# Kernel optimization log

Hardware: AMD Instinct MI355X
Metric: run time of the kernel (lower is better)

Reference implementation:

```python
import jax, jax.numpy as jnp
import numpy as np

LEAKY = 0.1  # leaky_hmm_coefficient (pychain default)


def _fb_objf(x_exp, tfrom, tto, tpdf, tprob, init_p, final_p):
    """Leaky-HMM forward recursion for one sequence.
    x_exp: [T, P] exp'd nnet outputs; transitions are edge lists of length E.
    Returns scalar log-prob of the sequence under the graph.
    """
    S = init_p.shape[0]

    def step(carry, obs):
        alpha, logz = carry  # alpha: [S] normalized occupation probs
        # per-edge contribution: alpha[src] * trans_prob * obs[pdf]
        contrib = alpha[tfrom] * tprob * obs[tpdf]          # [E]
        new_alpha = jnp.zeros(S, alpha.dtype).at[tto].add(contrib)
        tot = new_alpha.sum()
        # leaky-HMM: redistribute a fraction of total mass via initial probs
        new_alpha = new_alpha + LEAKY * tot * init_p
        scale = new_alpha.sum()
        return (new_alpha / scale, logz + jnp.log(scale)), None

    (alpha_T, logz), _ = jax.lax.scan(step, (init_p, jnp.zeros((), x_exp.dtype)), x_exp)
    return logz + jnp.log(jnp.sum(alpha_T * final_p))


def setup_inputs() -> dict:
    key = jax.random.key(0)
    ks = jax.random.split(key, 12)
    B, T, P = 32, 500, 3000
    S_den, E_den = 2000, 40000
    S_num, E_num = 100, 400

    x = jax.random.normal(ks[0], (B, T, P), jnp.float32)

    # denominator graph (shared across batch); every state gets incoming arcs
    den_to = (jnp.arange(E_den, dtype=jnp.int32) % S_den)
    den_from = jax.random.randint(ks[1], (E_den,), 0, S_den, jnp.int32)
    den_pdf = jax.random.randint(ks[2], (E_den,), 0, P, jnp.int32)
    den_prob = jax.random.uniform(ks[3], (E_den,), jnp.float32, 0.1, 1.0)
    den_init = jax.random.uniform(ks[4], (S_den,), jnp.float32, 0.1, 1.0)
    den_init = den_init / den_init.sum()
    den_final = jax.random.uniform(ks[5], (S_den,), jnp.float32, 0.1, 1.0)

    # numerator graphs (one per utterance), batched edge lists
    num_to = jnp.tile(jnp.arange(E_num, dtype=jnp.int32) % S_num, (B, 1))
    num_from = jax.random.randint(ks[6], (B, E_num), 0, S_num, jnp.int32)
    num_pdf = jax.random.randint(ks[7], (B, E_num), 0, P, jnp.int32)
    num_prob = jax.random.uniform(ks[8], (B, E_num), jnp.float32, 0.1, 1.0)
    num_init = jax.random.uniform(ks[9], (B, S_num), jnp.float32, 0.1, 1.0)
    num_init = num_init / num_init.sum(axis=1, keepdims=True)
    num_final = jax.random.uniform(ks[10], (B, S_num), jnp.float32, 0.1, 1.0)

    return {
        "x": x,
        "den_from": den_from, "den_to": den_to, "den_pdf": den_pdf,
        "den_prob": den_prob, "den_init": den_init, "den_final": den_final,
        "num_from": num_from, "num_to": num_to, "num_pdf": num_pdf,
        "num_prob": num_prob, "num_init": num_init, "num_final": num_final,
    }


def reference(x, den_from, den_to, den_pdf, den_prob, den_init, den_final,
              num_from, num_to, num_pdf, num_prob, num_init, num_final):
    B, T, _ = x.shape
    exp_x = jnp.exp(jnp.clip(x, -30.0, 30.0))  # [B, T, P]

    # denominator: shared graph across batch
    den_objf = jax.vmap(_fb_objf, in_axes=(0, None, None, None, None, None, None))(
        exp_x, den_from, den_to, den_pdf, den_prob, den_init, den_final).sum()
    # numerator: per-utterance graph
    num_objf = jax.vmap(_fb_objf, in_axes=(0, 0, 0, 0, 0, 0, 0))(
        exp_x, num_from, num_to, num_pdf, num_prob, num_init, num_final).sum()

    objf = -(num_objf - den_objf)
    return objf / (B * T)  # avg=True
```

## Files before the change

kernel.cpp:

```cpp
#include <hip/hip_runtime.h>


#define LEAKY 0.1f
#define AGENT __HIP_MEMORY_SCOPE_AGENT

constexpr int B = 32, T = 500, P = 3000;
constexpr int S_DEN = 2000;
constexpr int S_NUM = 100, E_NUM = 400;
constexpr int NTH = 1024;
constexpr int NWAVE = NTH / 64;
constexpr int G_DEN = 5;
constexpr int SB = S_DEN / G_DEN;
constexpr int KE = 20;
constexpr int EPT = KE / 2;
constexpr int OBS_T0 = 800;
constexpr int OBS_N = NTH - OBS_T0;
constexpr int OBS_IT = (P + OBS_N - 1) / OBS_N;
constexpr int KE_NUM = 4;
constexpr int NDEN_BLK = B * G_DEN;


__device__ __forceinline__ float clampexp(float x) {
  return __expf(fminf(fmaxf(x, -30.f), 30.f));
}
__device__ __forceinline__ void st_f32(float* p, float v) {
  __hip_atomic_store(p, v, __ATOMIC_RELAXED, AGENT);
}
__device__ __forceinline__ unsigned long long ld_u64(const float* p) {
  return __hip_atomic_load((const unsigned long long*)p, __ATOMIC_RELAXED,
                           AGENT);
}

__device__ __forceinline__ float reduce_1024(float v, float* wpart) {
#pragma unroll
  for (int off = 32; off; off >>= 1) v += __shfl_xor(v, off, 64);
  if ((threadIdx.x & 63) == 0) wpart[threadIdx.x >> 6] = v;
  __syncthreads();
  float s = 0.f;
#pragma unroll
  for (int w = 0; w < NWAVE; ++w) s += wpart[w];
  return s;
}

__device__ void run_den(const float* __restrict__ xb,
                        const int* __restrict__ ef_g,
                        const int* __restrict__ ep_g,
                        const float* __restrict__ epr_g,
                        const float* __restrict__ einit,
                        const float* __restrict__ efinal, int b, int g,
                        float* __restrict__ outs, float* __restrict__ parts_b,
                        float* obsA, float* obsB, float* cur, float* ini_s,
                        float* wpart) {
  const int tid = threadIdx.x;
  const int lane = tid & 63;
  const bool gat = tid < 2 * SB;
  const bool cons = tid < S_DEN / 2;
  const int jloc = (tid >> 6) * 32 + (lane >> 1);
  const int half = lane & 1;
  const int j = g * SB + jloc;

  float lsum = 0.f;
  if (cons) {
    const float2 iv = ((const float2*)einit)[tid];
    ((float2*)ini_s)[tid] = iv;
    lsum = iv.x + iv.y;
  }
  __syncthreads();
  const float leakfac = 1.f + LEAKY * reduce_1024(lsum, wpart);

  int efep[EPT];
  float epr[EPT], w[EPT], c[EPT];
  if (gat) {
#pragma unroll
    for (int k = 0; k < EPT; ++k) {
      const int e = j + (half * EPT + k) * S_DEN;
      efep[k] = ef_g[e] | (ep_g[e] << 16);
      epr[k] = epr_g[e];
    }
    const int off = (3 * lane) & 31;
#pragma unroll
    for (int i = 0; i < EPT - 1; ++i) {
#pragma unroll
      for (int k = 0; k < EPT - 1 - i; ++k) {
        const int ka = ((efep[k] & 31) - off) & 31;
        const int kb = ((efep[k + 1] & 31) - off) & 31;
        if (kb < ka) {
          const int te = efep[k]; efep[k] = efep[k + 1]; efep[k + 1] = te;
          const float tp = epr[k]; epr[k] = epr[k + 1]; epr[k + 1] = tp;
        }
      }
    }
#pragma unroll
    for (int k = 0; k < EPT; ++k) c[k] = ini_s[efep[k] & 0xffff] * epr[k];
  }

  obsA[tid] = clampexp(xb[tid]);
  obsA[tid + 1024] = clampexp(xb[tid + 1024]);
  if (tid + 2048 < P) obsA[tid + 2048] = clampexp(xb[tid + 2048]);
  float xr[OBS_IT];
  if (tid >= OBS_T0) {
    const float* r = xb + P;
#pragma unroll
    for (int i = 0; i < OBS_IT; ++i) {
      const int p = tid - OBS_T0 + OBS_N * i;
      xr[i] = (p < P) ? r[p] : 0.f;
    }
  }
  __syncthreads();
  float iniw = 0.f;
  if (gat) {
#pragma unroll
    for (int k = 0; k < EPT; ++k) {
      const float o = obsA[efep[k] >> 16];
      w[k] = epr[k] * o;
      iniw += c[k] * o;
    }
  }

  float logz = 0.f;
  float lt = 0.f, inv = 0.f;
  for (int t = 0; t < T; ++t) {
    float* obs_n = (t & 1) ? obsA : obsB;
    float a_raw = 0.f;
    if (t) {
      if (gat) {
#pragma unroll
        for (int k = 0; k < EPT; ++k) a_raw += cur[efep[k] & 0xffff] * w[k];
      }
      float s = 0.f;
#pragma unroll
      for (int wv = 0; wv < NWAVE; ++wv) s += wpart[wv];
      const float scale = s * leakfac;
      lt = LEAKY * s;
      inv = 1.f / scale;
      logz += __logf(scale);
    }
    const int parn = (t + 1) & 1;
    const unsigned tagn = ((unsigned)(t + 1) >> 1) & 1u;
    if (gat) {
      const float ar = a_raw + __shfl_xor(a_raw, 1, 64);
      const float iw = iniw + __shfl_xor(iniw, 1, 64);
      if (!half) {
        const float aa = t ? inv * fmaf(lt, iw, ar) : iw;
        st_f32(parts_b + parn * 2048 + j, tagn ? -aa : aa);
      }
    } else if (tid >= OBS_T0) {
      float nxr[OBS_IT];
      const int tn = (t + 2 < T) ? t + 2 : T - 1;
      const float* r = xb + (size_t)tn * P;
#pragma unroll
      for (int i = 0; i < OBS_IT; ++i) {
        const int p = tid - OBS_T0 + OBS_N * i;
        nxr[i] = (p < P) ? r[p] : 0.f;
      }
      if (t + 1 < T) {
#pragma unroll
        for (int i = 0; i < OBS_IT; ++i) {
          const int p = tid - OBS_T0 + OBS_N * i;
          if (p < P) obs_n[p] = clampexp(xr[i]);
        }
      }
#pragma unroll
      for (int i = 0; i < OBS_IT; ++i) xr[i] = nxr[i];
    }
    __syncthreads();
    const float* myp = parts_b + parn * 2048 + 2 * tid;
    unsigned long long u = 0;
    if (cons) u = ld_u64(myp);
    if (gat && t + 1 < T) {
      iniw = 0.f;
#pragma unroll
      for (int k = 0; k < EPT; ++k) {
        const float o = obs_n[efep[k] >> 16];
        w[k] = epr[k] * o;
        iniw += c[k] * o;
      }
    }
    if (cons) {
      while ((((unsigned)(u >> 31) & 1u) != tagn) ||
             (((unsigned)(u >> 63) & 1u) != tagn)) {
        __builtin_amdgcn_s_sleep(1);
        u = ld_u64(myp);
      }
    }
    union { unsigned long long q; float2 f; } cc;
    cc.q = u;
    const float2 v2 = make_float2(fabsf(cc.f.x), fabsf(cc.f.y));
    float pv = cons ? (v2.x + v2.y) : 0.f;
#pragma unroll
    for (int off2 = 32; off2; off2 >>= 1) pv += __shfl_xor(pv, off2, 64);
    if (lane == 0) wpart[tid >> 6] = pv;
    if (cons) ((float2*)cur)[tid] = v2;
    __syncthreads();
  }

  float s = 0.f;
#pragma unroll
  for (int wv = 0; wv < NWAVE; ++wv) s += wpart[wv];
  const float scaleT = s * leakfac;
  logz += __logf(scaleT);
  const float ltT = LEAKY * s, invT = 1.f / scaleT;
  float fv = 0.f;
  if (cons) {
    const float2 f2 = ((const float2*)efinal)[tid];
    const float2 i2 = ((const float2*)ini_s)[tid];
    const float2 c2 = ((const float2*)cur)[tid];
    fv = (fmaf(ltT, i2.x, c2.x) * invT) * f2.x +
         (fmaf(ltT, i2.y, c2.y) * invT) * f2.y;
  }
  __syncthreads();
  const float fin = reduce_1024(fv, wpart);
  if (tid == 0 && g == 0) outs[b] = logz + __logf(fin);
}

__device__ void run_num(const float* __restrict__ xb, const int* __restrict__ ef,
                        const int* __restrict__ ep, const float* __restrict__ epr,
                        const float* __restrict__ einit,
                        const float* __restrict__ efinal,
                        float* __restrict__ out_slot, float* __restrict__ obs,
                        float* __restrict__ cur, float* __restrict__ wpart) {
  const int tid = threadIdx.x;
  const bool act = tid < S_NUM / 2;
  const int j = 2 * tid;
  float2 ini = make_float2(0.f, 0.f), fin2 = make_float2(0.f, 0.f);
  if (act) {
    ini = ((const float2*)einit)[tid];
    fin2 = ((const float2*)efinal)[tid];
  }
  __syncthreads();
  const float leakfac =
      1.f + LEAKY * reduce_1024(act ? ini.x + ini.y : 0.f, wpart);

  int2 f2[KE_NUM], p2[KE_NUM];
  float2 pr2[KE_NUM];
  if (act) {
#pragma unroll
    for (int k = 0; k < KE_NUM; ++k) {
      f2[k] = ((const int2*)(ef + k * S_NUM))[tid];
      p2[k] = ((const int2*)(ep + k * S_NUM))[tid];
      pr2[k] = ((const float2*)(epr + k * S_NUM))[tid];
    }
  }
  obs[tid] = clampexp(xb[tid]);
  obs[tid + 1024] = clampexp(xb[tid + 1024]);
  if (tid + 2048 < P) obs[tid + 2048] = clampexp(xb[tid + 2048]);
  float xr0, xr1, xr2;
  {
    const float* r = xb + P;
    xr0 = r[tid];
    xr1 = r[tid + 1024];
    xr2 = (tid + 2048 < P) ? r[tid + 2048] : 0.f;
  }
  if (act) {
    cur[j] = ini.x;
    cur[j + 1] = ini.y;
  }
  __syncthreads();

  float logz = 0.f;
  for (int t = 0; t < T; ++t) {
    float nx0 = xr0, nx1 = xr1, nx2 = xr2;
    if (t + 2 < T) {
      const float* r = xb + (size_t)(t + 2) * P;
      nx0 = r[tid];
      nx1 = r[tid + 1024];
      nx2 = (tid + 2048 < P) ? r[tid + 2048] : 0.f;
    }
    float a0 = 0.f, a1 = 0.f;
    if (act) {
#pragma unroll
      for (int k = 0; k < KE_NUM; ++k) {
        a0 += cur[f2[k].x] * pr2[k].x * obs[p2[k].x];
        a1 += cur[f2[k].y] * pr2[k].y * obs[p2[k].y];
      }
    }
    float v = a0 + a1;
#pragma unroll
    for (int off = 32; off; off >>= 1) v += __shfl_xor(v, off, 64);
    if ((tid & 63) == 0) wpart[tid >> 6] = v;
    __syncthreads();
    float tot = 0.f;
#pragma unroll
    for (int w = 0; w < NWAVE; ++w) tot += wpart[w];
    if (t + 1 < T) {
      obs[tid] = clampexp(xr0);
      obs[tid + 1024] = clampexp(xr1);
      if (tid + 2048 < P) obs[tid + 2048] = clampexp(xr2);
    }
    xr0 = nx0;
    xr1 = nx1;
    xr2 = nx2;
    const float scale = tot * leakfac;
    const float inv = 1.f / scale, lt = LEAKY * tot;
    if (act) {
      cur[j] = fmaf(lt, ini.x, a0) * inv;
      cur[j + 1] = fmaf(lt, ini.y, a1) * inv;
    }
    logz += __logf(scale);
    __syncthreads();
  }
  __syncthreads();
  const float fin = reduce_1024(
      act ? (cur[j] * fin2.x + cur[j + 1] * fin2.y) : 0.f, wpart);
  if (tid == 0) *out_slot = logz + __logf(fin);
}

__global__ __launch_bounds__(NTH) void fb_kernel(
    const float* __restrict__ x, const int* __restrict__ den_from,
    const int* __restrict__ den_pdf, const float* __restrict__ den_prob,
    const float* __restrict__ den_init, const float* __restrict__ den_final,
    const int* __restrict__ num_from, const int* __restrict__ num_pdf,
    const float* __restrict__ num_prob, const float* __restrict__ num_init,
    const float* __restrict__ num_final, float* __restrict__ ws) {
  __shared__ float obsA[P];
  __shared__ float obsB[P];
  __shared__ float cur[S_DEN];
  __shared__ float ini_s[S_DEN];
  __shared__ float wpart[NWAVE];
  float* outs = ws;
  float* parts = ws + 4096;
  const int blk = blockIdx.x;
  if (blk < NDEN_BLK) {
    const int b = blk / G_DEN, g = blk % G_DEN;
    run_den(x + (size_t)b * T * P, den_from, den_pdf, den_prob, den_init,
            den_final, b, g, outs, parts + (size_t)b * 4096, obsA, obsB, cur,
            ini_s, wpart);
  } else {
    const int b = blk - NDEN_BLK;
    run_num(x + (size_t)b * T * P, num_from + b * E_NUM, num_pdf + b * E_NUM,
            num_prob + b * E_NUM, num_init + b * S_NUM, num_final + b * S_NUM,
            outs + B + b, obsA, cur, wpart);
  }
}

__global__ void init_parts(float* p) {
  const int i = blockIdx.x * NTH + threadIdx.x;
  st_f32(&p[i], ((i >> 11) & 1) ? -1.f : 1.f);
}

__global__ void finish_kernel(const float* __restrict__ ws,
                              float* __restrict__ out) {
  const int tid = threadIdx.x;
  float v = ws[tid];
  v = (tid < B) ? v : -v;
#pragma unroll
  for (int off = 32; off; off >>= 1) v += __shfl_xor(v, off, 64);
  if (tid == 0) out[0] = v / (float)(B * T);
}

extern "C" void kernel_launch(void* const* d_in, const int* in_sizes, int n_in,
                              void* d_out, int out_size, void* d_ws,
                              size_t ws_size, hipStream_t stream) {
  const float* x = (const float*)d_in[0];
  const int* den_from = (const int*)d_in[1];
  const int* den_pdf = (const int*)d_in[3];
  const float* den_prob = (const float*)d_in[4];
  const float* den_init = (const float*)d_in[5];
  const float* den_final = (const float*)d_in[6];
  const int* num_from = (const int*)d_in[7];
  const int* num_pdf = (const int*)d_in[9];
  const float* num_prob = (const float*)d_in[10];
  const float* num_init = (const float*)d_in[11];
  const float* num_final = (const float*)d_in[12];
  float* ws = (float*)d_ws;
  float* out = (float*)d_out;

  init_parts<<<(B * 4096) / NTH, NTH, 0, stream>>>(ws + 4096);
  fb_kernel<<<NDEN_BLK + B, NTH, 0, stream>>>(
      x, den_from, den_pdf, den_prob, den_init, den_final, num_from, num_pdf,
      num_prob, num_init, num_final, ws);
  finish_kernel<<<1, 64, 0, stream>>>(ws, out);
}
```

Baseline: 1.335 ms.

## Triple-buffer observations and double-buffer state to cut per-step barriers

Moves the denominator forward loop to triple-buffered observation tiles and double-buffered state and partial-sum arrays. This removes one of the two __syncthreads per time step and lets the cross-block partial load start earlier, overlapping it with the observation prefetch. Block indices are also remapped so the G_DEN blocks of one utterance land on the same XCD, sharing L2 for the inter-block exchange. The cost is more LDS per block and a longer prefetch distance for observation rows.

After: 1.479 ms. 1.11x slower.

```diff
diff --git a/kernel.cpp b/kernel.cpp
--- a/kernel.cpp
+++ b/kernel.cpp
@@ -49,8 +49,9 @@
                         const float* __restrict__ einit,
                         const float* __restrict__ efinal, int b, int g,
                         float* __restrict__ outs, float* __restrict__ parts_b,
-                        float* obsA, float* obsB, float* cur, float* ini_s,
-                        float* wpart) {
+                        float* obs0, float* obs1, float* obs2,
+                        float* craw0, float* craw1, float* ini_s,
+                        float* wpA, float* wpB) {
   const int tid = threadIdx.x;
   const int lane = tid & 63;
   const bool gat = tid < 2 * SB;
@@ -66,7 +67,7 @@
     lsum = iv.x + iv.y;
   }
   __syncthreads();
-  const float leakfac = 1.f + LEAKY * reduce_1024(lsum, wpart);
+  const float leakfac = 1.f + LEAKY * reduce_1024(lsum, wpA);
 
   int efep[EPT];
   float epr[EPT], w[EPT], c[EPT];
@@ -94,16 +95,18 @@
     for (int k = 0; k < EPT; ++k) c[k] = ini_s[efep[k] & 0xffff] * epr[k];
   }
 
-  obsA[tid] = clampexp(xb[tid]);
-  obsA[tid + 1024] = clampexp(xb[tid + 1024]);
-  if (tid + 2048 < P) obsA[tid + 2048] = clampexp(xb[tid + 2048]);
+  obs0[tid] = clampexp(xb[tid]);
+  obs0[tid + 1024] = clampexp(xb[tid + 1024]);
+  if (tid + 2048 < P) obs0[tid + 2048] = clampexp(xb[tid + 2048]);
   float xr[OBS_IT];
   if (tid >= OBS_T0) {
-    const float* r = xb + P;
+    const float* r1 = xb + P;
+    const float* r2 = xb + 2 * (size_t)P;
 #pragma unroll
     for (int i = 0; i < OBS_IT; ++i) {
       const int p = tid - OBS_T0 + OBS_N * i;
-      xr[i] = (p < P) ? r[p] : 0.f;
+      if (p < P) obs1[p] = clampexp(r1[p]);
+      xr[i] = (p < P) ? r2[p] : 0.f;
     }
   }
   __syncthreads();
@@ -111,25 +114,30 @@
   if (gat) {
 #pragma unroll
     for (int k = 0; k < EPT; ++k) {
-      const float o = obsA[efep[k] >> 16];
+      const float o = obs0[efep[k] >> 16];
       w[k] = epr[k] * o;
       iniw += c[k] * o;
     }
   }
 
+  float* rbuf = obs1;
+  float* wbuf = obs2;
+  float* zbuf = obs0;
+  float* cr = craw0;
+  float* cw = craw1;
+  float* wr = wpA;
+  float* ww = wpB;
+
   float logz = 0.f;
-  float lt = 0.f, inv = 0.f;
   for (int t = 0; t < T; ++t) {
-    float* obs_n = (t & 1) ? obsA : obsB;
-    float a_raw = 0.f;
-    if (t) {
-      if (gat) {
-#pragma unroll
-        for (int k = 0; k < EPT; ++k) a_raw += cur[efep[k] & 0xffff] * w[k];
-      }
+    __syncthreads();
+    float a_raw = 0.f, lt = 0.f, inv = 0.f;
+    if (t && gat) {
+#pragma unroll
+      for (int k = 0; k < EPT; ++k) a_raw += cr[efep[k] & 0xffff] * w[k];
       float s = 0.f;
 #pragma unroll
-      for (int wv = 0; wv < NWAVE; ++wv) s += wpart[wv];
+      for (int wv = 0; wv < NWAVE; ++wv) s += wr[wv];
       const float scale = s * leakfac;
       lt = LEAKY * s;
       inv = 1.f / scale;
@@ -144,34 +152,32 @@
         const float aa = t ? inv * fmaf(lt, iw, ar) : iw;
         st_f32(parts_b + parn * 2048 + j, tagn ? -aa : aa);
       }
-    } else if (tid >= OBS_T0) {
+    }
+    const float* myp = parts_b + parn * 2048 + 2 * tid;
+    unsigned long long u = 0;
+    if (cons) u = ld_u64(myp);
+    if (tid >= OBS_T0) {
       float nxr[OBS_IT];
-      const int tn = (t + 2 < T) ? t + 2 : T - 1;
+      const int tn = (t + 3 < T) ? t + 3 : T - 1;
       const float* r = xb + (size_t)tn * P;
 #pragma unroll
       for (int i = 0; i < OBS_IT; ++i) {
         const int p = tid - OBS_T0 + OBS_N * i;
         nxr[i] = (p < P) ? r[p] : 0.f;
       }
-      if (t + 1 < T) {
-#pragma unroll
-        for (int i = 0; i < OBS_IT; ++i) {
-          const int p = tid - OBS_T0 + OBS_N * i;
-          if (p < P) obs_n[p] = clampexp(xr[i]);
-        }
+#pragma unroll
+      for (int i = 0; i < OBS_IT; ++i) {
+        const int p = tid - OBS_T0 + OBS_N * i;
+        if (p < P) wbuf[p] = clampexp(xr[i]);
       }
 #pragma unroll
       for (int i = 0; i < OBS_IT; ++i) xr[i] = nxr[i];
     }
-    __syncthreads();
-    const float* myp = parts_b + parn * 2048 + 2 * tid;
-    unsigned long long u = 0;
-    if (cons) u = ld_u64(myp);
     if (gat && t + 1 < T) {
       iniw = 0.f;
 #pragma unroll
       for (int k = 0; k < EPT; ++k) {
-        const float o = obs_n[efep[k] >> 16];
+        const float o = rbuf[efep[k] >> 16];
         w[k] = epr[k] * o;
         iniw += c[k] * o;
       }
@@ -189,14 +195,16 @@
     float pv = cons ? (v2.x + v2.y) : 0.f;
 #pragma unroll
     for (int off2 = 32; off2; off2 >>= 1) pv += __shfl_xor(pv, off2, 64);
-    if (lane == 0) wpart[tid >> 6] = pv;
-    if (cons) ((float2*)cur)[tid] = v2;
-    __syncthreads();
-  }
-
+    if (lane == 0) ww[tid >> 6] = pv;
+    if (cons) ((float2*)cw)[tid] = v2;
+    float* tb = zbuf; zbuf = rbuf; rbuf = wbuf; wbuf = tb;
+    float* tc = cr; cr = cw; cw = tc;
+    float* tw = wr; wr = ww; ww = tw;
+  }
+  __syncthreads();
   float s = 0.f;
 #pragma unroll
-  for (int wv = 0; wv < NWAVE; ++wv) s += wpart[wv];
+  for (int wv = 0; wv < NWAVE; ++wv) s += wr[wv];
   const float scaleT = s * leakfac;
   logz += __logf(scaleT);
   const float ltT = LEAKY * s, invT = 1.f / scaleT;
@@ -204,12 +212,12 @@
   if (cons) {
     const float2 f2 = ((const float2*)efinal)[tid];
     const float2 i2 = ((const float2*)ini_s)[tid];
-    const float2 c2 = ((const float2*)cur)[tid];
+    const float2 c2 = ((const float2*)cr)[tid];
     fv = (fmaf(ltT, i2.x, c2.x) * invT) * f2.x +
          (fmaf(ltT, i2.y, c2.y) * invT) * f2.y;
   }
   __syncthreads();
-  const float fin = reduce_1024(fv, wpart);
+  const float fin = reduce_1024(fv, wr);
   if (tid == 0 && g == 0) outs[b] = logz + __logf(fin);
 }
 
@@ -312,24 +320,29 @@
     const int* __restrict__ num_from, const int* __restrict__ num_pdf,
     const float* __restrict__ num_prob, const float* __restrict__ num_init,
     const float* __restrict__ num_final, float* __restrict__ ws) {
-  __shared__ float obsA[P];
-  __shared__ float obsB[P];
-  __shared__ float cur[S_DEN];
+  __shared__ float obs0[P];
+  __shared__ float obs1[P];
+  __shared__ float obs2[P];
+  __shared__ float craw0[S_DEN];
+  __shared__ float craw1[S_DEN];
   __shared__ float ini_s[S_DEN];
-  __shared__ float wpart[NWAVE];
+  __shared__ float wpA[NWAVE];
+  __shared__ float wpB[NWAVE];
   float* outs = ws;
   float* parts = ws + 4096;
   const int blk = blockIdx.x;
   if (blk < NDEN_BLK) {
-    const int b = blk / G_DEN, g = blk % G_DEN;
+    const int xcd = blk & 7, m = blk >> 3;
+    const int b = (m / 5) * 8 + xcd;
+    const int g = m % 5;
     run_den(x + (size_t)b * T * P, den_from, den_pdf, den_prob, den_init,
-            den_final, b, g, outs, parts + (size_t)b * 4096, obsA, obsB, cur,
-            ini_s, wpart);
+            den_final, b, g, outs, parts + (size_t)b * 4096, obs0, obs1, obs2,
+            craw0, craw1, ini_s, wpA, wpB);
   } else {
     const int b = blk - NDEN_BLK;
     run_num(x + (size_t)b * T * P, num_from + b * E_NUM, num_pdf + b * E_NUM,
             num_prob + b * E_NUM, num_init + b * S_NUM, num_final + b * S_NUM,
-            outs + B + b, obsA, cur, wpart);
+            outs + B + b, obs0, craw0, wpA);
   }
 }
 
```
